# Optimization experiments

Hardware: AMD Instinct MI355X
Metric: run time of the kernel (lower is better)

Reference implementation:

```python
import jax, jax.numpy as jnp
import numpy as np

N = 100000   # nodes
E = 1600000  # edges (before self-loops)
D = 128      # in_feats
H = 128      # n_hidden


def setup_inputs() -> dict:
    key = jax.random.key(0)
    k = jax.random.split(key, 6)
    x = jax.random.normal(k[0], (N, D), dtype=jnp.float32)
    src = jax.random.randint(k[1], (E,), 0, N, dtype=jnp.int32)
    dst = jax.random.randint(k[2], (E,), 0, N, dtype=jnp.int32)
    W1 = jax.random.normal(k[3], (D, H), dtype=jnp.float32) / np.float32(np.sqrt(D))
    b1 = jnp.zeros((H,), jnp.float32)
    W2 = jax.random.normal(k[4], (H, H), dtype=jnp.float32) / np.float32(np.sqrt(H))
    b2 = jnp.zeros((H,), jnp.float32)
    return {"x": x, "src": src, "dst": dst, "W1": W1, "b1": b1, "W2": W2, "b2": b2}


def _gcn(x, src, dst, W1, b1, W2, b2):
    n = x.shape[0]
    # add_self_loop(g)
    loops = jnp.arange(n, dtype=src.dtype)
    s = jnp.concatenate([src, loops])
    d = jnp.concatenate([dst, loops])
    ones = jnp.ones((s.shape[0],), dtype=x.dtype)
    deg_out = jax.ops.segment_sum(ones, s, num_segments=n)  # src out-degree
    deg_in = jax.ops.segment_sum(ones, d, num_segments=n)   # dst in-degree
    # DGL GraphConv norm='both': D_out^{-1/2} on source side, D_in^{-1/2} on dest side
    norm_out = jax.lax.rsqrt(jnp.maximum(deg_out, 1.0))[:, None]
    norm_in = jax.lax.rsqrt(jnp.maximum(deg_in, 1.0))[:, None]

    def layer(h, W, b):
        h = h * norm_out                                   # [n, f]
        agg = jax.ops.segment_sum(h[s], d, num_segments=n)  # gather + scatter-add over edges
        return (agg * norm_in) @ W + b

    h = layer(x, W1, b1)
    # dropout p=0 -> identity
    h = layer(h, W2, b2)
    return h


def reference(x, src, dst, W1, b1, W2, b2):
    return _gcn(x, src, dst, W1, b1, W2, b2)
```

## Files before the change

### kernel.cpp

```cpp
#include <hip/hip_runtime.h>

#define FD 128
#define SHIFT 10
#define BNODES 1024
#define NBK 128
#define CHUNK 4096
#define ST 512

typedef unsigned int u32;
typedef unsigned short u16;
typedef unsigned char u8;
typedef __attribute__((ext_vector_type(8))) short short8;
typedef __attribute__((ext_vector_type(4))) float f32x4;
typedef __attribute__((ext_vector_type(4))) u32 u32x4;

__device__ inline u16 f2bf(float f) {
  u32 u = __float_as_uint(f);
  u += 0x7fffu + ((u >> 16) & 1u);
  return (u16)(u >> 16);
}
__device__ inline float bf2f(u16 h) { return __uint_as_float((u32)h << 16); }

__global__ __launch_bounds__(512) void k_hist(const int* __restrict__ src,
                                              const int* __restrict__ dst,
                                              int* __restrict__ bcntD,
                                              int* __restrict__ bcntS,
                                              int e, int n, int nbuck) {
  __shared__ int shD[NBK];
  __shared__ int shS[NBK];
  int tid = threadIdx.x;
  if (tid < NBK) { shD[tid] = 0; shS[tid] = 0; }
  __syncthreads();
  int total = e + n;
  for (int t = blockIdx.x * blockDim.x + tid; t < total; t += gridDim.x * blockDim.x) {
    if (t < e) {
      atomicAdd(&shD[dst[t] >> SHIFT], 1);
      atomicAdd(&shS[src[t] >> SHIFT], 1);
    } else {
      atomicAdd(&shD[(t - e) >> SHIFT], 1);
    }
  }
  __syncthreads();
  if (tid < nbuck) {
    if (shD[tid]) atomicAdd(&bcntD[tid], shD[tid]);
    if (shS[tid]) atomicAdd(&bcntS[tid], shS[tid]);
  }
}

__global__ __launch_bounds__(NBK) void k_bscan(
    const int* __restrict__ bcntD, const int* __restrict__ bcntS,
    int* __restrict__ bbaseD, int* __restrict__ bcurD,
    int* __restrict__ bbaseS, int* __restrict__ bcurS,
    int nbuck, int totalD, int totalS) {
  __shared__ int shD[NBK];
  __shared__ int shS[NBK];
  int tid = threadIdx.x;
  int vD = (tid < nbuck) ? bcntD[tid] : 0;
  int vS = (tid < nbuck) ? bcntS[tid] : 0;
  shD[tid] = vD; shS[tid] = vS;
  __syncthreads();
  for (int off = 1; off < NBK; off <<= 1) {
    int aD = (tid >= off) ? shD[tid - off] : 0;
    int aS = (tid >= off) ? shS[tid - off] : 0;
    __syncthreads();
    shD[tid] += aD; shS[tid] += aS;
    __syncthreads();
  }
  if (tid < nbuck) {
    int exD = shD[tid] - vD; bbaseD[tid] = exD; bcurD[tid] = exD;
    int exS = shS[tid] - vS; bbaseS[tid] = exS; bcurS[tid] = exS;
  }
  if (tid == 0) { bbaseD[nbuck] = totalD; bbaseS[nbuck] = totalS; }
}

__global__ __launch_bounds__(ST) void k_scatter(
    const int* __restrict__ src, const int* __restrict__ dst,
    int* __restrict__ bcurD, int* __restrict__ bcurS,
    u32* __restrict__ pairs, u16* __restrict__ pairs2,
    int e, int n, int nbuck) {
  __shared__ int histD[NBK], exclD[NBK], gbaseD[NBK], rankD[NBK];
  __shared__ int histS[NBK], exclS[NBK], gbaseS[NBK], rankS[NBK];
  __shared__ u32 stgv[CHUNK];
  __shared__ u8  stgb[CHUNK];
  __shared__ u16 stg2[CHUNK];
  __shared__ u8  stg2b[CHUNK];
  int tid = threadIdx.x;
  int c0 = blockIdx.x * CHUNK;
  int total = e + n;
  if (tid < NBK) { histD[tid] = 0; histS[tid] = 0; }
  __syncthreads();
  u32 pv_[8]; int bD_[8], bS_[8]; bool v_[8], vs_[8];
  #pragma unroll
  for (int i = 0; i < 8; ++i) {
    int t = c0 + i * ST + tid;
    v_[i] = (t < total);
    vs_[i] = (t < e);
    pv_[i] = 0; bD_[i] = 0; bS_[i] = 0;
    if (v_[i]) {
      int s, d;
      if (vs_[i]) { s = src[t]; d = dst[t]; }
      else        { s = t - e;  d = s; }
      pv_[i] = ((u32)(d & (BNODES - 1)) << 22) | (u32)s;
      bD_[i] = d >> SHIFT;
      atomicAdd(&histD[bD_[i]], 1);
      if (vs_[i]) { bS_[i] = s >> SHIFT; atomicAdd(&histS[bS_[i]], 1); }
    }
  }
  __syncthreads();
  int hD = 0, hS = 0;
  if (tid < NBK) { hD = histD[tid]; hS = histS[tid]; }
  __syncthreads();
  for (int off = 1; off < NBK; off <<= 1) {
    int aD = 0, aS = 0;
    if (tid < NBK && tid >= off) { aD = histD[tid - off]; aS = histS[tid - off]; }
    __syncthreads();
    if (tid < NBK) { histD[tid] += aD; histS[tid] += aS; }
    __syncthreads();
  }
  if (tid < NBK) {
    int exD = histD[tid] - hD; exclD[tid] = exD; rankD[tid] = exD;
    int exS = histS[tid] - hS; exclS[tid] = exS; rankS[tid] = exS;
    gbaseD[tid] = (tid < nbuck && hD > 0) ? atomicAdd(&bcurD[tid], hD) : 0;
    gbaseS[tid] = (tid < nbuck && hS > 0) ? atomicAdd(&bcurS[tid], hS) : 0;
  }
  __syncthreads();
  #pragma unroll
  for (int i = 0; i < 8; ++i) {
    if (v_[i]) {
      int p = atomicAdd(&rankD[bD_[i]], 1);
      stgv[p] = pv_[i];
      stgb[p] = (u8)bD_[i];
    }
    if (vs_[i]) {
      int p = atomicAdd(&rankS[bS_[i]], 1);
      stg2[p] = (u16)(pv_[i] & (BNODES - 1));
      stg2b[p] = (u8)bS_[i];
    }
  }
  __syncthreads();
  int V = min(CHUNK, total - c0);
  for (int j = tid; j < V; j += ST) {
    int b = stgb[j];
    pairs[gbaseD[b] + (j - exclD[b])] = stgv[j];
  }
  int V2 = min(CHUNK, e - c0);
  for (int j = tid; j < V2; j += ST) {
    int b = stg2b[j];
    pairs2[gbaseS[b] + (j - exclS[b])] = stg2[j];
  }
}

__global__ __launch_bounds__(1024) void k_build(
    const u32* __restrict__ pairs, const int* __restrict__ bbase,
    const u16* __restrict__ pairs2, const int* __restrict__ bbaseS,
    int* __restrict__ rp, int* __restrict__ col,
    float* __restrict__ nin, float* __restrict__ nout,
    int n, int nbuck, int total) {
  __shared__ int cnt[BNODES];
  __shared__ int off_[BNODES];
  __shared__ int cur[BNODES];
  int tid = threadIdx.x;
  if (blockIdx.x >= (unsigned)nbuck) {
    int b = blockIdx.x - nbuck;
    int base = bbaseS[b], end = bbaseS[b + 1];
    cnt[tid] = 0;
    __syncthreads();
    for (int t = base + tid; t < end; t += 1024)
      atomicAdd(&cnt[(int)pairs2[t]], 1);
    __syncthreads();
    int node = (b << SHIFT) + tid;
    if (node < n) nout[node] = rsqrtf((float)(cnt[tid] + 1));
    return;
  }
  int b = blockIdx.x;
  int base = bbase[b], end = bbase[b + 1];
  int node0 = b << SHIFT;
  cnt[tid] = 0;
  __syncthreads();
  for (int t = base + tid; t < end; t += 1024)
    atomicAdd(&cnt[(int)(pairs[t] >> 22)], 1);
  __syncthreads();
  int c = cnt[tid];
  off_[tid] = c;
  __syncthreads();
  for (int off = 1; off < BNODES; off <<= 1) {
    int add = (tid >= off) ? off_[tid - off] : 0;
    __syncthreads();
    off_[tid] += add;
    __syncthreads();
  }
  int ex = off_[tid] - c;
  int node = node0 + tid;
  if (node < n) {
    rp[node] = base + ex;
    nin[node] = rsqrtf((float)c);
  }
  if (b == nbuck - 1 && tid == 0) rp[n] = total;
  cur[tid] = ex;
  __syncthreads();
  for (int t = base + tid; t < end; t += 1024) {
    u32 pr = pairs[t];
    int p = atomicAdd(&cur[(int)(pr >> 22)], 1);
    col[base + p] = (int)(pr & 0x3FFFFFu);
  }
}

__global__ void k_prepw(const float* __restrict__ W1, u32* __restrict__ wf1hi,
                        u32* __restrict__ wf1lo,
                        const float* __restrict__ W2, u32* __restrict__ wf2hi,
                        u32* __restrict__ wf2lo) {
  int gi = blockIdx.x * 256 + threadIdx.x;
  int i = gi & 8191;
  const float* W = (gi < 8192) ? W1 : W2;
  u32* wfhi = (gi < 8192) ? wf1hi : wf2hi;
  u32* wflo = (gi < 8192) ? wf1lo : wf2lo;
  int m = i & 3, l = (i >> 2) & 63, f = i >> 8;
  int kt = f & 3, nt = f >> 2;
  int k0 = kt * 32 + ((l >> 4) << 3) + 2 * m;
  int c = nt * 16 + (l & 15);
  float w0 = W[k0 * FD + c], w1 = W[(k0 + 1) * FD + c];
  u16 h0 = f2bf(w0), h1 = f2bf(w1);
  u16 l0 = f2bf(w0 - bf2f(h0)), l1 = f2bf(w1 - bf2f(h1));
  wfhi[i] = (u32)h0 | ((u32)h1 << 16);
  wflo[i] = (u32)l0 | ((u32)l1 << 16);
}

__global__ __launch_bounds__(256) void k_gemmx(
    const float* __restrict__ x,
    const u32* __restrict__ wfhi, const u32* __restrict__ wflo,
    u32* __restrict__ tout, int n) {
  __shared__ u32 As[4096];
  int tid = threadIdx.x;
  int lane = tid & 63;
  int mt = tid >> 6;
  int r0 = blockIdx.x * 64;

  #pragma unroll
  for (int it = 0; it < 16; ++it) {
    int w = it * 256 + tid;
    int row = w >> 6, u = w & 63;
    int grow = r0 + row;
    float2 v = make_float2(0.f, 0.f);
    if (grow < n) v = *(const float2*)(x + (size_t)grow * FD + u * 2);
    As[row * 64 + (u ^ ((row & 7) << 2))] = (u32)f2bf(v.x) | ((u32)f2bf(v.y) << 16);
  }
  __syncthreads();

  short8 afh[4];
  int arow = mt * 16 + (lane & 15);
  #pragma unroll
  for (int kt = 0; kt < 4; ++kt) {
    int boff = arow * 256 + ((kt * 64 + (lane >> 4) * 16) ^ ((arow & 7) << 4));
    afh[kt] = *(const short8*)((const char*)As + boff);
  }
  __syncthreads();

  for (int nt = 0; nt < 8; ++nt) {
    f32x4 oacc = {0.f, 0.f, 0.f, 0.f};
    #pragma unroll
    for (int kt = 0; kt < 4; ++kt) {
      int f = nt * 4 + kt;
      short8 wh = *(const short8*)(wfhi + (size_t)(f * 64 + lane) * 4);
      short8 wl = *(const short8*)(wflo + (size_t)(f * 64 + lane) * 4);
      oacc = __builtin_amdgcn_mfma_f32_16x16x32_bf16(afh[kt], wh, oacc, 0, 0, 0);
      oacc = __builtin_amdgcn_mfma_f32_16x16x32_bf16(afh[kt], wl, oacc, 0, 0, 0);
    }
    int c = nt * 16 + (lane & 15);
    #pragma unroll
    for (int j = 0; j < 4; ++j) {
      int lrow = mt * 16 + (lane >> 4) * 4 + j;
      ((u16*)As)[lrow * 128 + c] = f2bf(oacc[j]);
    }
  }
  __syncthreads();
  #pragma unroll
  for (int it = 0; it < 4; ++it) {
    int ci = it * 256 + tid;
    int lrow = ci >> 4, chk = ci & 15;
    int row = r0 + lrow;
    if (row < n)
      *(u32x4*)(tout + (size_t)row * 64 + chk * 4) =
          *(const u32x4*)(As + lrow * 64 + chk * 4);
  }
}

__global__ __launch_bounds__(256) void k_scale(
    const u32* __restrict__ t1, const float* __restrict__ nout,
    u32* __restrict__ y1, int n) {
  int tot = (n + 1) * 64;
  for (int idx = blockIdx.x * blockDim.x + threadIdx.x; idx < tot;
       idx += gridDim.x * blockDim.x) {
    int row = idx >> 6;
    if (row >= n) { y1[idx] = 0; continue; }
    float w = nout[row];
    u32 v = t1[idx];
    float lo = __uint_as_float(v << 16) * w;
    float hi = __uint_as_float(v & 0xFFFF0000u) * w;
    y1[idx] = (u32)f2bf(lo) | ((u32)f2bf(hi) << 16);
  }
}

__global__ __launch_bounds__(256) void k_agg(
    const u32* __restrict__ hs, const int* __restrict__ rp,
    const int* __restrict__ col, const float* __restrict__ nin,
    const float* __restrict__ bias,
    float* __restrict__ fout, u32* __restrict__ hsout, int n, int mode) {
  int wid = (blockIdx.x * 256 + threadIdx.x) >> 6;
  int lane = threadIdx.x & 63;
  int g = lane >> 4, ch = lane & 15;
  int r = wid * 4 + g;
  bool valid = (r < n);
  int e0 = 0, e1 = 0;
  if (valid) { e0 = rp[r]; e1 = rp[r + 1]; }
  int m = e1 - e0;
  m = max(m, __shfl_xor(m, 16, 64));
  m = max(m, __shfl_xor(m, 32, 64));
  int trips = (m + 7) >> 3;
  float acc[8] = {0.f, 0.f, 0.f, 0.f, 0.f, 0.f, 0.f, 0.f};
  const u32x4* hv = (const u32x4*)hs;
  int em1 = (e1 > 0) ? (e1 - 1) : 0;
  for (int it = 0; it < trips; ++it) {
    int tb = e0 + it * 8;
    u32x4 buf[8];
    #pragma unroll
    for (int u = 0; u < 8; ++u) {
      int idx = tb + u;
      int s = col[min(idx, em1)];
      s = (idx < e1) ? s : n;
      buf[u] = hv[(size_t)s * 16 + ch];
    }
    #pragma unroll
    for (int u = 0; u < 8; ++u)
      #pragma unroll
      for (int j = 0; j < 4; ++j) {
        u32 x = buf[u][j];
        acc[2 * j]     += __uint_as_float(x << 16);
        acc[2 * j + 1] += __uint_as_float(x & 0xFFFF0000u);
      }
  }
  if (!valid) return;
  float wi = nin[r];
  float4 b0 = *(const float4*)(bias + ch * 8);
  float4 b1v = *(const float4*)(bias + ch * 8 + 4);
  float v[8];
  v[0] = acc[0] * wi + b0.x;  v[1] = acc[1] * wi + b0.y;
  v[2] = acc[2] * wi + b0.z;  v[3] = acc[3] * wi + b0.w;
  v[4] = acc[4] * wi + b1v.x; v[5] = acc[5] * wi + b1v.y;
  v[6] = acc[6] * wi + b1v.z; v[7] = acc[7] * wi + b1v.w;
  if (mode == 0) {
    *(float4*)(fout + (size_t)r * FD + ch * 8)     = make_float4(v[0], v[1], v[2], v[3]);
    *(float4*)(fout + (size_t)r * FD + ch * 8 + 4) = make_float4(v[4], v[5], v[6], v[7]);
  } else {
    u32 hi[4];
    #pragma unroll
    for (int j = 0; j < 4; ++j)
      hi[j] = (u32)f2bf(v[2 * j]) | ((u32)f2bf(v[2 * j + 1]) << 16);
    int sch = ch ^ (r & 7);
    u32x4 hq = {hi[0], hi[1], hi[2], hi[3]};
    *(u32x4*)(hsout + (size_t)r * 64 + sch * 4) = hq;
  }
}

__global__ __launch_bounds__(256) void k_gemm2(
    const u32* __restrict__ ahi,
    const u32* __restrict__ wfhi, const u32* __restrict__ wflo,
    const float* __restrict__ nout, u32* __restrict__ yout, int n) {
  __shared__ u32 As[4096];
  int tid = threadIdx.x;
  int lane = tid & 63;
  int mt = tid >> 6;
  int r0 = blockIdx.x * 64;

  const u32x4* gh = (const u32x4*)(ahi + (size_t)r0 * 64);
  u32x4* sh_ = (u32x4*)As;
  #pragma unroll
  for (int t = 0; t < 4; ++t) sh_[t * 256 + tid] = gh[t * 256 + tid];
  __syncthreads();

  short8 afh[4];
  int arow = mt * 16 + (lane & 15);
  #pragma unroll
  for (int kt = 0; kt < 4; ++kt) {
    int boff = arow * 256 + ((kt * 64 + (lane >> 4) * 16) ^ ((arow & 7) << 4));
    afh[kt] = *(const short8*)((const char*)As + boff);
  }
  __syncthreads();

  float wout[4];
  #pragma unroll
  for (int j = 0; j < 4; ++j) {
    int row = r0 + mt * 16 + (lane >> 4) * 4 + j;
    wout[j] = (row < n) ? nout[row] : 0.f;
  }

  for (int nt = 0; nt < 8; ++nt) {
    f32x4 oacc = {0.f, 0.f, 0.f, 0.f};
    #pragma unroll
    for (int kt = 0; kt < 4; ++kt) {
      int f = nt * 4 + kt;
      short8 wh = *(const short8*)(wfhi + (size_t)(f * 64 + lane) * 4);
      short8 wl = *(const short8*)(wflo + (size_t)(f * 64 + lane) * 4);
      oacc = __builtin_amdgcn_mfma_f32_16x16x32_bf16(afh[kt], wh, oacc, 0, 0, 0);
      oacc = __builtin_amdgcn_mfma_f32_16x16x32_bf16(afh[kt], wl, oacc, 0, 0, 0);
    }
    int c = nt * 16 + (lane & 15);
    #pragma unroll
    for (int j = 0; j < 4; ++j) {
      int lrow = mt * 16 + (lane >> 4) * 4 + j;
      ((u16*)As)[lrow * 128 + c] = f2bf(oacc[j] * wout[j]);
    }
  }
  __syncthreads();
  #pragma unroll
  for (int it = 0; it < 4; ++it) {
    int ci = it * 256 + tid;
    int lrow = ci >> 4, chk = ci & 15;
    int row = r0 + lrow;
    if (row < n)
      *(u32x4*)(yout + (size_t)row * 64 + chk * 4) =
          *(const u32x4*)(As + lrow * 64 + chk * 4);
  }
}

extern "C" void kernel_launch(void* const* d_in, const int* in_sizes, int n_in,
                              void* d_out, int out_size, void* d_ws, size_t ws_size,
                              hipStream_t stream) {
  const float* x  = (const float*)d_in[0];
  const int* src  = (const int*)d_in[1];
  const int* dst  = (const int*)d_in[2];
  const float* W1 = (const float*)d_in[3];
  const float* b1 = (const float*)d_in[4];
  const float* W2 = (const float*)d_in[5];
  const float* b2 = (const float*)d_in[6];
  float* out = (float*)d_out;

  int n = in_sizes[0] / FD;
  int e = in_sizes[1];
  int total = e + n;
  int nbuck = (n + BNODES - 1) >> SHIFT;

  char* ws = (char*)d_ws;
  size_t off = 0;
  auto alloc = [&](size_t bytes) -> void* {
    void* p = ws + off;
    off += (bytes + 255) / 256 * 256;
    return p;
  };
  u32* bufA  = (u32*)alloc((size_t)(n + 16) * 64 * 4);
  u32* t1bf  = bufA;
  u32* y2    = bufA;
  u32* bufB  = (u32*)alloc((size_t)(n + 16) * 64 * 4);
  u32* pairs = bufB;
  u32* y1    = bufB;
  u32* bufC  = (u32*)alloc((size_t)(n + 64) * 64 * 4);
  u16* pairs2 = (u16*)bufC;
  u32* h1bf  = bufC;
  int* col   = (int*)alloc((size_t)total * 4 + 256);
  int* rp    = (int*)alloc((size_t)(n + 1) * 4);
  float* nin  = (float*)alloc((size_t)n * 4);
  float* nout = (float*)alloc((size_t)n * 4);
  int* bcntD  = (int*)alloc(NBK * 4);
  int* bcntS  = (int*)alloc(NBK * 4);
  int* bbaseD = (int*)alloc((NBK + 1) * 4);
  int* bbaseS = (int*)alloc((NBK + 1) * 4);
  int* bcurD  = (int*)alloc(NBK * 4);
  int* bcurS  = (int*)alloc(NBK * 4);
  u32* wf1hi  = (u32*)alloc(8192 * 4);
  u32* wf1lo  = (u32*)alloc(8192 * 4);
  u32* wf2hi  = (u32*)alloc(8192 * 4);
  u32* wf2lo  = (u32*)alloc(8192 * 4);

  hipMemsetAsync(bcntD, 0, (size_t)NBK * 4 * 2, stream);
  hipMemsetAsync(bufA + (size_t)n * 64, 0, 64 * 4, stream);

  int ggrid = (n + 63) / 64;
  k_prepw<<<64, 256, 0, stream>>>(W1, wf1hi, wf1lo, W2, wf2hi, wf2lo);
  k_gemmx<<<ggrid, 256, 0, stream>>>(x, wf1hi, wf1lo, t1bf, n);

  k_hist<<<256, 512, 0, stream>>>(src, dst, bcntD, bcntS, e, n, nbuck);
  k_bscan<<<1, NBK, 0, stream>>>(bcntD, bcntS, bbaseD, bcurD, bbaseS, bcurS,
                                 nbuck, total, e);
  k_scatter<<<(total + CHUNK - 1) / CHUNK, ST, 0, stream>>>(
      src, dst, bcurD, bcurS, pairs, pairs2, e, n, nbuck);
  k_build<<<2 * nbuck, 1024, 0, stream>>>(pairs, bbaseD, pairs2, bbaseS,
                                          rp, col, nin, nout, n, nbuck, total);

  k_scale<<<2048, 256, 0, stream>>>(t1bf, nout, y1, n);

  int agrid = (n + 15) / 16;
  k_agg<<<agrid, 256, 0, stream>>>(y1, rp, col, nin, b1, nullptr, h1bf, n, 1);
  k_gemm2<<<ggrid, 256, 0, stream>>>(h1bf, wf2hi, wf2lo, nout, y2, n);
  k_agg<<<agrid, 256, 0, stream>>>(y2, rp, col, nin, b2, out, nullptr, n, 0);
}
```

Baseline: 244.5 us.

## Fuse weight prep into histogram and x-GEMM into edge scatter launches

Weight splitting into bf16 hi/lo fragments now runs as extra blocks of the histogram kernel, and the first-layer x@W1 GEMM runs as extra blocks of the edge bucket-scatter kernel, each GEMM block handling two 64-row tiles in shared memory. This removes two kernel launches and lets independent graph-build and GEMM work overlap on the GPU. The CSR build's 1024-element block scan is replaced with a wavefront shuffle scan plus a small cross-wave scan, cutting many barriers. The risk is that the scatter blocks get heavier shared-memory footprints, and mixing block types can cause load imbalance.

```diff
diff --git a/kernel.cpp b/kernel.cpp
--- a/kernel.cpp
+++ b/kernel.cpp
@@ -21,18 +21,35 @@
 }
 __device__ inline float bf2f(u16 h) { return __uint_as_float((u32)h << 16); }
 
-__global__ __launch_bounds__(512) void k_hist(const int* __restrict__ src,
-                                              const int* __restrict__ dst,
-                                              int* __restrict__ bcntD,
-                                              int* __restrict__ bcntS,
-                                              int e, int n, int nbuck) {
+__global__ __launch_bounds__(512) void k_histpw(
+    const int* __restrict__ src, const int* __restrict__ dst,
+    int* __restrict__ bcntD, int* __restrict__ bcntS, int e, int n, int nbuck,
+    const float* __restrict__ W1, u32* __restrict__ wf1hi, u32* __restrict__ wf1lo,
+    const float* __restrict__ W2, u32* __restrict__ wf2hi, u32* __restrict__ wf2lo) {
+  int tid = threadIdx.x;
+  if (blockIdx.x >= 256) {
+    int gi = (blockIdx.x - 256) * 512 + tid;
+    int i = gi & 8191;
+    const float* W = (gi < 8192) ? W1 : W2;
+    u32* wfhi = (gi < 8192) ? wf1hi : wf2hi;
+    u32* wflo = (gi < 8192) ? wf1lo : wf2lo;
+    int m = i & 3, l = (i >> 2) & 63, f = i >> 8;
+    int kt = f & 3, nt = f >> 2;
+    int k0 = kt * 32 + ((l >> 4) << 3) + 2 * m;
+    int c = nt * 16 + (l & 15);
+    float w0 = W[k0 * FD + c], w1 = W[(k0 + 1) * FD + c];
+    u16 h0 = f2bf(w0), h1 = f2bf(w1);
+    u16 l0 = f2bf(w0 - bf2f(h0)), l1 = f2bf(w1 - bf2f(h1));
+    wfhi[i] = (u32)h0 | ((u32)h1 << 16);
+    wflo[i] = (u32)l0 | ((u32)l1 << 16);
+    return;
+  }
   __shared__ int shD[NBK];
   __shared__ int shS[NBK];
-  int tid = threadIdx.x;
   if (tid < NBK) { shD[tid] = 0; shS[tid] = 0; }
   __syncthreads();
   int total = e + n;
-  for (int t = blockIdx.x * blockDim.x + tid; t < total; t += gridDim.x * blockDim.x) {
+  for (int t = blockIdx.x * 512 + tid; t < total; t += 256 * 512) {
     if (t < e) {
       atomicAdd(&shD[dst[t] >> SHIFT], 1);
       atomicAdd(&shS[src[t] >> SHIFT], 1);
@@ -73,18 +90,87 @@
   if (tid == 0) { bbaseD[nbuck] = totalD; bbaseS[nbuck] = totalS; }
 }
 
-__global__ __launch_bounds__(ST) void k_scatter(
+__global__ __launch_bounds__(ST) void k_scatgx(
     const int* __restrict__ src, const int* __restrict__ dst,
     int* __restrict__ bcurD, int* __restrict__ bcurS,
     u32* __restrict__ pairs, u16* __restrict__ pairs2,
-    int e, int n, int nbuck) {
-  __shared__ int histD[NBK], exclD[NBK], gbaseD[NBK], rankD[NBK];
-  __shared__ int histS[NBK], exclS[NBK], gbaseS[NBK], rankS[NBK];
-  __shared__ u32 stgv[CHUNK];
-  __shared__ u8  stgb[CHUNK];
-  __shared__ u16 stg2[CHUNK];
-  __shared__ u8  stg2b[CHUNK];
-  int tid = threadIdx.x;
+    int e, int n, int nbuck, int nsc,
+    const float* __restrict__ x,
+    const u32* __restrict__ wfhi, const u32* __restrict__ wflo,
+    u32* __restrict__ tout) {
+  __shared__ __align__(16) u8 smem[36864];
+  int tid512 = threadIdx.x;
+
+  if (blockIdx.x >= (unsigned)nsc) {
+    int u = tid512 >> 8, tid = tid512 & 255;
+    u32* Au = (u32*)smem + u * 4096;
+    int lane = tid & 63;
+    int mt = tid >> 6;
+    int r0 = ((blockIdx.x - nsc) * 2 + u) * 64;
+
+    #pragma unroll
+    for (int it = 0; it < 16; ++it) {
+      int w = it * 256 + tid;
+      int row = w >> 6, uu = w & 63;
+      int grow = r0 + row;
+      float2 v = make_float2(0.f, 0.f);
+      if (grow < n) v = *(const float2*)(x + (size_t)grow * FD + uu * 2);
+      Au[row * 64 + (uu ^ ((row & 7) << 2))] = (u32)f2bf(v.x) | ((u32)f2bf(v.y) << 16);
+    }
+    __syncthreads();
+
+    short8 afh[4];
+    int arow = mt * 16 + (lane & 15);
+    #pragma unroll
+    for (int kt = 0; kt < 4; ++kt) {
+      int boff = arow * 256 + ((kt * 64 + (lane >> 4) * 16) ^ ((arow & 7) << 4));
+      afh[kt] = *(const short8*)((const char*)Au + boff);
+    }
+    __syncthreads();
+
+    for (int nt = 0; nt < 8; ++nt) {
+      f32x4 oacc = {0.f, 0.f, 0.f, 0.f};
+      #pragma unroll
+      for (int kt = 0; kt < 4; ++kt) {
+        int f = nt * 4 + kt;
+        short8 wh = *(const short8*)(wfhi + (size_t)(f * 64 + lane) * 4);
+        short8 wl = *(const short8*)(wflo + (size_t)(f * 64 + lane) * 4);
+        oacc = __builtin_amdgcn_mfma_f32_16x16x32_bf16(afh[kt], wh, oacc, 0, 0, 0);
+        oacc = __builtin_amdgcn_mfma_f32_16x16x32_bf16(afh[kt], wl, oacc, 0, 0, 0);
+      }
+      int c = nt * 16 + (lane & 15);
+      #pragma unroll
+      for (int j = 0; j < 4; ++j) {
+        int lrow = mt * 16 + (lane >> 4) * 4 + j;
+        ((u16*)Au)[lrow * 128 + c] = f2bf(oacc[j]);
+      }
+    }
+    __syncthreads();
+    #pragma unroll
+    for (int it = 0; it < 4; ++it) {
+      int ci = it * 256 + tid;
+      int lrow = ci >> 4, chk = ci & 15;
+      int row = r0 + lrow;
+      if (row < n)
+        *(u32x4*)(tout + (size_t)row * 64 + chk * 4) =
+            *(const u32x4*)(Au + lrow * 64 + chk * 4);
+    }
+    return;
+  }
+
+  int* histD = (int*)smem;
+  int* exclD = histD + NBK;
+  int* gbaseD = exclD + NBK;
+  int* rankD = gbaseD + NBK;
+  int* histS = rankD + NBK;
+  int* exclS = histS + NBK;
+  int* gbaseS = exclS + NBK;
+  int* rankS = gbaseS + NBK;
+  u32* stgv = (u32*)(smem + 4096);
+  u16* stg2 = (u16*)(smem + 20480);
+  u8*  stgb = smem + 28672;
+  u8*  stg2b = smem + 32768;
+  int tid = tid512;
   int c0 = blockIdx.x * CHUNK;
   int total = e + n;
   if (tid < NBK) { histD[tid] = 0; histS[tid] = 0; }
@@ -157,8 +243,8 @@
     float* __restrict__ nin, float* __restrict__ nout,
     int n, int nbuck, int total) {
   __shared__ int cnt[BNODES];
-  __shared__ int off_[BNODES];
   __shared__ int cur[BNODES];
+  __shared__ int wsum[16];
   int tid = threadIdx.x;
   if (blockIdx.x >= (unsigned)nbuck) {
     int b = blockIdx.x - nbuck;
@@ -181,15 +267,27 @@
     atomicAdd(&cnt[(int)(pairs[t] >> 22)], 1);
   __syncthreads();
   int c = cnt[tid];
-  off_[tid] = c;
-  __syncthreads();
-  for (int off = 1; off < BNODES; off <<= 1) {
-    int add = (tid >= off) ? off_[tid - off] : 0;
-    __syncthreads();
-    off_[tid] += add;
-    __syncthreads();
-  }
-  int ex = off_[tid] - c;
+  int lane = tid & 63, wv = tid >> 6;
+  int v = c;
+  #pragma unroll
+  for (int o = 1; o < 64; o <<= 1) {
+    int t = __shfl_up(v, o, 64);
+    if (lane >= o) v += t;
+  }
+  if (lane == 63) wsum[wv] = v;
+  __syncthreads();
+  if (tid < 16) {
+    int w = wsum[tid];
+    #pragma unroll
+    for (int o = 1; o < 16; o <<= 1) {
+      int t = __shfl_up(w, o, 64);
+      if (lane >= o) w += t;
+    }
+    wsum[tid] = w;
+  }
+  __syncthreads();
+  int incl = v + (wv ? wsum[wv - 1] : 0);
+  int ex = incl - c;
   int node = node0 + tid;
   if (node < n) {
     rp[node] = base + ex;
@@ -202,85 +300,6 @@
     u32 pr = pairs[t];
     int p = atomicAdd(&cur[(int)(pr >> 22)], 1);
     col[base + p] = (int)(pr & 0x3FFFFFu);
-  }
-}
-
-__global__ void k_prepw(const float* __restrict__ W1, u32* __restrict__ wf1hi,
-                        u32* __restrict__ wf1lo,
-                        const float* __restrict__ W2, u32* __restrict__ wf2hi,
-                        u32* __restrict__ wf2lo) {
-  int gi = blockIdx.x * 256 + threadIdx.x;
-  int i = gi & 8191;
-  const float* W = (gi < 8192) ? W1 : W2;
-  u32* wfhi = (gi < 8192) ? wf1hi : wf2hi;
-  u32* wflo = (gi < 8192) ? wf1lo : wf2lo;
-  int m = i & 3, l = (i >> 2) & 63, f = i >> 8;
-  int kt = f & 3, nt = f >> 2;
-  int k0 = kt * 32 + ((l >> 4) << 3) + 2 * m;
-  int c = nt * 16 + (l & 15);
-  float w0 = W[k0 * FD + c], w1 = W[(k0 + 1) * FD + c];
-  u16 h0 = f2bf(w0), h1 = f2bf(w1);
-  u16 l0 = f2bf(w0 - bf2f(h0)), l1 = f2bf(w1 - bf2f(h1));
-  wfhi[i] = (u32)h0 | ((u32)h1 << 16);
-  wflo[i] = (u32)l0 | ((u32)l1 << 16);
-}
-
-__global__ __launch_bounds__(256) void k_gemmx(
-    const float* __restrict__ x,
-    const u32* __restrict__ wfhi, const u32* __restrict__ wflo,
-    u32* __restrict__ tout, int n) {
-  __shared__ u32 As[4096];
-  int tid = threadIdx.x;
-  int lane = tid & 63;
-  int mt = tid >> 6;
-  int r0 = blockIdx.x * 64;
-
-  #pragma unroll
-  for (int it = 0; it < 16; ++it) {
-    int w = it * 256 + tid;
-    int row = w >> 6, u = w & 63;
-    int grow = r0 + row;
-    float2 v = make_float2(0.f, 0.f);
-    if (grow < n) v = *(const float2*)(x + (size_t)grow * FD + u * 2);
-    As[row * 64 + (u ^ ((row & 7) << 2))] = (u32)f2bf(v.x) | ((u32)f2bf(v.y) << 16);
-  }
-  __syncthreads();
-
-  short8 afh[4];
-  int arow = mt * 16 + (lane & 15);
-  #pragma unroll
-  for (int kt = 0; kt < 4; ++kt) {
-    int boff = arow * 256 + ((kt * 64 + (lane >> 4) * 16) ^ ((arow & 7) << 4));
-    afh[kt] = *(const short8*)((const char*)As + boff);
-  }
-  __syncthreads();
-
-  for (int nt = 0; nt < 8; ++nt) {
-    f32x4 oacc = {0.f, 0.f, 0.f, 0.f};
-    #pragma unroll
-    for (int kt = 0; kt < 4; ++kt) {
-      int f = nt * 4 + kt;
-      short8 wh = *(const short8*)(wfhi + (size_t)(f * 64 + lane) * 4);
-      short8 wl = *(const short8*)(wflo + (size_t)(f * 64 + lane) * 4);
-      oacc = __builtin_amdgcn_mfma_f32_16x16x32_bf16(afh[kt], wh, oacc, 0, 0, 0);
-      oacc = __builtin_amdgcn_mfma_f32_16x16x32_bf16(afh[kt], wl, oacc, 0, 0, 0);
-    }
-    int c = nt * 16 + (lane & 15);
-    #pragma unroll
-    for (int j = 0; j < 4; ++j) {
-      int lrow = mt * 16 + (lane >> 4) * 4 + j;
-      ((u16*)As)[lrow * 128 + c] = f2bf(oacc[j]);
-    }
-  }
-  __syncthreads();
-  #pragma unroll
-  for (int it = 0; it < 4; ++it) {
-    int ci = it * 256 + tid;
-    int lrow = ci >> 4, chk = ci & 15;
-    int row = r0 + lrow;
-    if (row < n)
-      *(u32x4*)(tout + (size_t)row * 64 + chk * 4) =
-          *(const u32x4*)(As + lrow * 64 + chk * 4);
   }
 }
 
@@ -473,21 +492,20 @@
   hipMemsetAsync(bcntD, 0, (size_t)NBK * 4 * 2, stream);
   hipMemsetAsync(bufA + (size_t)n * 64, 0, 64 * 4, stream);
 
-  int ggrid = (n + 63) / 64;
-  k_prepw<<<64, 256, 0, stream>>>(W1, wf1hi, wf1lo, W2, wf2hi, wf2lo);
-  k_gemmx<<<ggrid, 256, 0, stream>>>(x, wf1hi, wf1lo, t1bf, n);
-
-  k_hist<<<256, 512, 0, stream>>>(src, dst, bcntD, bcntS, e, n, nbuck);
+  k_histpw<<<288, 512, 0, stream>>>(src, dst, bcntD, bcntS, e, n, nbuck,
+                                    W1, wf1hi, wf1lo, W2, wf2hi, wf2lo);
   k_bscan<<<1, NBK, 0, stream>>>(bcntD, bcntS, bbaseD, bcurD, bbaseS, bcurS,
                                  nbuck, total, e);
-  k_scatter<<<(total + CHUNK - 1) / CHUNK, ST, 0, stream>>>(
-      src, dst, bcurD, bcurS, pairs, pairs2, e, n, nbuck);
+  int nsc = (total + CHUNK - 1) / CHUNK;
+  int ngx = (n + 127) / 128;
+  k_scatgx<<<nsc + ngx, ST, 0, stream>>>(src, dst, bcurD, bcurS, pairs, pairs2,
+                                         e, n, nbuck, nsc, x, wf1hi, wf1lo, t1bf);
   k_build<<<2 * nbuck, 1024, 0, stream>>>(pairs, bbaseD, pairs2, bbaseS,
                                           rp, col, nin, nout, n, nbuck, total);
-
   k_scale<<<2048, 256, 0, stream>>>(t1bf, nout, y1, n);
 
   int agrid = (n + 15) / 16;
+  int ggrid = (n + 63) / 64;
   k_agg<<<agrid, 256, 0, stream>>>(y1, rp, col, nin, b1, nullptr, h1bf, n, 1);
   k_gemm2<<<ggrid, 256, 0, stream>>>(h1bf, wf2hi, wf2lo, nout, y2, n);
   k_agg<<<agrid, 256, 0, stream>>>(y2, rp, col, nin, b2, out, nullptr, n, 0);
```

New measurement: 232.7 us. -4.8%, faster.
